# Optimization experiments

Hardware: AMD Instinct MI355X
Metric: run time of the kernel (lower is better)

The kernel has to match this reference:

```python
import jax, jax.numpy as jnp
import numpy as np

# Deformable Conv v2 (modulated) config matching init_kwargs
KH, KW = 3, 3
STRIDE = (1, 1)
PAD = (1, 1)
DIL = (1, 1)


def _deform_conv2d(input, offset, mask, weight, bias):
    """Modulated deformable conv2d (DCNv2), deformable_groups=1.

    input:  [B, C, H, W]
    offset: [B, 2*K, Ho, Wo]  (y, x) interleaved per kernel tap
    mask:   [B, K, Ho, Wo]
    weight: [O, C, KH, KW]
    bias:   [O]
    """
    B, C, H, W = input.shape
    O = weight.shape[0]
    K = KH * KW
    sh, sw = STRIDE
    ph, pw = PAD
    dh, dw = DIL
    Ho = (H + 2 * ph - dh * (KH - 1) - 1) // sh + 1
    Wo = (W + 2 * pw - dw * (KW - 1) - 1) // sw + 1
    dt = input.dtype

    # Base sampling grid per kernel tap: [K, Ho, Wo] (broadcasted)
    ky, kx = jnp.meshgrid(jnp.arange(KH), jnp.arange(KW), indexing='ij')
    ky = ky.reshape(K).astype(dt)
    kx = kx.reshape(K).astype(dt)
    base_y = (jnp.arange(Ho, dtype=dt) * sh - ph)[None, :, None] + (ky * dh)[:, None, None]
    base_x = (jnp.arange(Wo, dtype=dt) * sw - pw)[None, None, :] + (kx * dw)[:, None, None]

    off = offset.reshape(B, K, 2, Ho, Wo)
    y = base_y[None] + off[:, :, 0]  # [B, K, Ho, Wo]
    x = base_x[None] + off[:, :, 1]

    y0 = jnp.floor(y)
    x0 = jnp.floor(x)
    wy = y - y0  # fractional parts
    wx = x - x0

    flat = input.reshape(B, C, H * W)

    def gather(yi, xi):
        # zero padding outside the image
        valid = ((yi >= 0) & (yi < H) & (xi >= 0) & (xi < W)).astype(dt)
        yc = jnp.clip(yi, 0, H - 1).astype(jnp.int32)
        xc = jnp.clip(xi, 0, W - 1).astype(jnp.int32)
        idx = (yc * W + xc).reshape(B, 1, K * Ho * Wo)
        v = jnp.take_along_axis(flat, jnp.broadcast_to(idx, (B, C, K * Ho * Wo)), axis=2)
        return v.reshape(B, C, K, Ho, Wo) * valid[:, None]

    g00 = gather(y0, x0)
    g01 = gather(y0, x0 + 1)
    g10 = gather(y0 + 1, x0)
    g11 = gather(y0 + 1, x0 + 1)

    wy = wy[:, None]  # [B, 1, K, Ho, Wo]
    wx = wx[:, None]
    val = (g00 * (1 - wy) * (1 - wx) + g01 * (1 - wy) * wx
           + g10 * wy * (1 - wx) + g11 * wy * wx)
    val = val * mask[:, None]  # modulation

    out = jnp.einsum('bckq,ock->boq', val.reshape(B, C, K, Ho * Wo),
                     weight.reshape(O, C, K))
    return out.reshape(B, O, Ho, Wo) + bias[None, :, None, None]


def setup_inputs() -> dict:
    key = jax.random.key(0)
    k1, k2, k3, k4, k5 = jax.random.split(key, 5)
    B, C, H, W = 8, 64, 96, 96
    O = 64
    K = KH * KW
    input = jax.random.normal(k1, (B, C, H, W), dtype=jnp.float32)
    offset = jax.random.normal(k2, (B, 2 * K, H, W), dtype=jnp.float32)
    mask = jax.random.uniform(k3, (B, K, H, W), dtype=jnp.float32)
    fan_in = C * KH * KW
    bound = 1.0 / np.sqrt(fan_in)
    weight = jax.random.uniform(k4, (O, C, KH, KW), minval=-bound, maxval=bound, dtype=jnp.float32)
    bias = jax.random.uniform(k5, (O,), minval=-bound, maxval=bound, dtype=jnp.float32)
    return {"input": input, "offset": offset, "mask": mask, "weight": weight, "bias": bias}


def reference(input, offset, mask, weight, bias):
    return _deform_conv2d(input, offset, mask, weight, bias)
```

## Files before the change

kernel.cpp:

```cpp
#include <hip/hip_runtime.h>
#include <stdint.h>

#define Hs 96
#define Ws 96
#define HW 9216

typedef _Float16 h2 __attribute__((ext_vector_type(2)));
typedef _Float16 f16x8 __attribute__((ext_vector_type(8)));
typedef float f32x4 __attribute__((ext_vector_type(4)));

__device__ __forceinline__ unsigned interp4(h2 w00, h2 w01, h2 w10, h2 w11,
                                            unsigned a, unsigned bq, unsigned c,
                                            unsigned d) {
  h2 r = w00 * __builtin_bit_cast(h2, a) + w01 * __builtin_bit_cast(h2, bq) +
         w10 * __builtin_bit_cast(h2, c) + w11 * __builtin_bit_cast(h2, d);
  return __builtin_bit_cast(unsigned, r);
}

__global__ __launch_bounds__(256) void k_transpose(const float* __restrict__ in,
                                                   _Float16* __restrict__ cl) {
  __shared__ _Float16 lt[32 * 68];
  int tid = threadIdx.x;
  int blk = blockIdx.x;
  int xt = blk % 3;
  int r = blk / 3;
  int y = r % Hs;
  int b = r / Hs;
  int x0 = xt * 32;
  {
    int xx = tid & 31, cc = tid >> 5;
    const float* src = in + (size_t)b * 64 * HW + y * Ws + x0 + xx;
#pragma unroll
    for (int i = 0; i < 8; ++i) {
      int c = cc * 8 + i;
      lt[xx * 68 + c] = (_Float16)src[(size_t)c * HW];
    }
  }
  __syncthreads();
  {
    int c4 = tid & 15, pg = tid >> 4;
    _Float16* dst = cl + ((size_t)(b * Hs + y) * Ws + x0) * 64 + c4 * 4;
#pragma unroll
    for (int i = 0; i < 2; ++i) {
      int x = pg * 2 + i;
      *(uint2*)(dst + (size_t)x * 64) = *(const uint2*)(lt + x * 68 + c4 * 4);
    }
  }
}

__global__ __launch_bounds__(576) void k_wconv(const float* __restrict__ w,
                                               _Float16* __restrict__ wg) {
  int o = blockIdx.x;
  int r = threadIdx.x;
  int t = r >> 6, c = r & 63;
  wg[((size_t)(t * 8 + (c >> 3)) * 64 + o) * 8 + (c & 7)] =
      (_Float16)w[(o * 64 + c) * 9 + t];
}

__device__ __forceinline__ void sample_tap(const char* inb,
                                           const unsigned* preA,
                                           const uint2* preW, uint4* vrow,
                                           int t, int g, int j) {
#pragma unroll
  for (int it = 0; it < 2; ++it) {
    int gg = g + it * 32;
    unsigned ax = preA[t * 64 + gg];
    uint2 pw = preW[t * 64 + gg];
    int a00 = (int)(ax & ~127u) + j * 16;
    int a01 = a00 + ((ax & 1) << 7);
    int a10 = a00 + ((ax & 2) * 6144);
    int a11 = a10 + ((ax & 1) << 7);
    h2 w00 = __builtin_bit_cast(h2, __builtin_amdgcn_perm(pw.x, pw.x, 0x01000100u));
    h2 w01 = __builtin_bit_cast(h2, __builtin_amdgcn_perm(pw.x, pw.x, 0x03020302u));
    h2 w10 = __builtin_bit_cast(h2, __builtin_amdgcn_perm(pw.y, pw.y, 0x01000100u));
    h2 w11 = __builtin_bit_cast(h2, __builtin_amdgcn_perm(pw.y, pw.y, 0x03020302u));
    uint4 g00 = *(const uint4*)(inb + a00);
    uint4 g01 = *(const uint4*)(inb + a01);
    uint4 g10 = *(const uint4*)(inb + a10);
    uint4 g11 = *(const uint4*)(inb + a11);
    uint4 o;
    o.x = interp4(w00, w01, w10, w11, g00.x, g01.x, g10.x, g11.x);
    o.y = interp4(w00, w01, w10, w11, g00.y, g01.y, g10.y, g11.y);
    o.z = interp4(w00, w01, w10, w11, g00.z, g01.z, g10.z, g11.z);
    o.w = interp4(w00, w01, w10, w11, g00.w, g01.w, g10.w, g11.w);
    vrow[gg * 9 + j] = o;
  }
}

__global__ __launch_bounds__(256, 5) void k_fused(
    const _Float16* __restrict__ incl, const float* __restrict__ off,
    const float* __restrict__ msk, const _Float16* __restrict__ wg,
    const float* __restrict__ bias, float* __restrict__ out) {
  __shared__ unsigned preA[576];
  __shared__ uint2 preW[576];
  __shared__ uint4 Vb[2][64 * 9];

  int tid = threadIdx.x;
  int blk = blockIdx.x;
  int b = blk & 7;
  int q0 = (blk >> 3) * 64;

  for (int i = tid; i < 576; i += 256) {
    int t = i >> 6, p = i & 63;
    int q = q0 + p;
    int qy = (int)(((unsigned)q * 43691u) >> 22);
    int qx = q - qy * 96;
    int ty = t / 3, tx = t - ty * 3;
    float dy = off[(size_t)(b * 18 + 2 * t) * HW + q];
    float dx = off[(size_t)(b * 18 + 2 * t + 1) * HW + q];
    float mv = msk[(size_t)(b * 9 + t) * HW + q];
    float yf = (float)(qy - 1 + ty) + dy;
    float xf = (float)(qx - 1 + tx) + dx;
    float y0f = floorf(yf), x0f = floorf(xf);
    float wy = yf - y0f, wx = xf - x0f;
    int y0 = (int)y0f, x0i = (int)x0f;
    int y1 = y0 + 1, x1 = x0i + 1;
    bool yv0 = (y0 >= 0) && (y0 < Hs);
    bool yv1 = (y1 >= 0) && (y1 < Hs);
    bool xv0 = (x0i >= 0) && (x0i < Ws);
    bool xv1 = (x1 >= 0) && (x1 < Ws);
    int y0c = min(max(y0, 0), Hs - 1), y1c = min(max(y1, 0), Hs - 1);
    int x0c = min(max(x0i, 0), Ws - 1), x1c = min(max(x1, 0), Ws - 1);
    float omy = 1.f - wy, omx = 1.f - wx;
    float f00 = omy * omx * mv * ((yv0 && xv0) ? 1.f : 0.f);
    float f01 = omy * wx  * mv * ((yv0 && xv1) ? 1.f : 0.f);
    float f10 = wy  * omx * mv * ((yv1 && xv0) ? 1.f : 0.f);
    float f11 = wy  * wx  * mv * ((yv1 && xv1) ? 1.f : 0.f);
    preA[i] = ((unsigned)(b * HW + y0c * 96 + x0c) * 128u) |
              (unsigned)(x1c - x0c) | ((unsigned)(y1c - y0c) << 1);
    uint2 pw;
    pw.x = __builtin_bit_cast(unsigned, __builtin_amdgcn_cvt_pkrtz(f00, f01));
    pw.y = __builtin_bit_cast(unsigned, __builtin_amdgcn_cvt_pkrtz(f10, f11));
    preW[i] = pw;
  }
  __syncthreads();

  int j = tid & 7;
  int g = tid >> 3;
  int lane = tid & 63, wv = tid >> 6;
  int n16 = lane & 15, q4 = lane >> 4;
  const char* inb = (const char*)incl;
  const uint4* Ag = (const uint4*)wg;

  f32x4 acc[4];
#pragma unroll
  for (int mt = 0; mt < 4; ++mt) {
    f32x4 z = {0.f, 0.f, 0.f, 0.f};
    acc[mt] = z;
  }

  sample_tap(inb, preA, preW, &Vb[0][0], 0, g, j);
  __syncthreads();

  for (int t = 0; t < 9; ++t) {
    int buf = t & 1;
    if (t < 8)
      sample_tap(inb, preA, preW, &Vb[buf ^ 1][0], t + 1, g, j);
#pragma unroll
    for (int kc = 0; kc < 2; ++kc) {
      f16x8 bfr = __builtin_bit_cast(
          f16x8, Vb[buf][(wv * 16 + n16) * 9 + kc * 4 + q4]);
#pragma unroll
      for (int mt = 0; mt < 4; ++mt) {
        f16x8 afr = __builtin_bit_cast(
            f16x8, Ag[(size_t)((t * 8 + kc * 4 + q4) * 64 + mt * 16 + n16)]);
        acc[mt] = __builtin_amdgcn_mfma_f32_16x16x32_f16(afr, bfr, acc[mt],
                                                         0, 0, 0);
      }
    }
    __syncthreads();
  }

  int colq = q0 + wv * 16 + n16;
  float* op = out + (size_t)b * 64 * HW + colq;
#pragma unroll
  for (int mt = 0; mt < 4; ++mt)
#pragma unroll
    for (int r = 0; r < 4; ++r) {
      int m = mt * 16 + q4 * 4 + r;
      op[(size_t)m * HW] = acc[mt][r] + bias[m];
    }
}

extern "C" void kernel_launch(void* const* d_in, const int* in_sizes, int n_in,
                              void* d_out, int out_size, void* d_ws, size_t ws_size,
                              hipStream_t stream) {
  const float* input = (const float*)d_in[0];
  const float* offset = (const float*)d_in[1];
  const float* mask = (const float*)d_in[2];
  const float* weight = (const float*)d_in[3];
  const float* bias = (const float*)d_in[4];
  float* out = (float*)d_out;

  _Float16* incl = (_Float16*)d_ws;
  _Float16* wg = (_Float16*)((char*)d_ws + 9437184);

  k_transpose<<<dim3(2304), dim3(256), 0, stream>>>(input, incl);
  k_wconv<<<dim3(64), dim3(576), 0, stream>>>(weight, wg);
  k_fused<<<dim3(1152), dim3(256), 0, stream>>>(incl, offset, mask, wg, bias, out);
}
```

Baseline: 108.8 us.

## Software-pipeline gathers in registers and repartition MFMA work by output channel

The fused kernel now issues the next tap's bilinear gather loads into registers right after the barrier, so they overlap the current tap's MFMA work. The interpolation is then done and stored to LDS at the start of the next iteration instead of immediately. The MFMA split changes from each wave owning 16 pixels across all 64 output channels to each wave owning 16 output channels across all 64 pixels. Weight fragments are prefetched one tap ahead and bias loads are hoisted. This costs more live registers (launch bounds drop from 5 to 4 blocks per CU) and adds LDS reads of the B fragments per wave.

```diff
diff --git a/kernel.cpp b/kernel.cpp
--- a/kernel.cpp
+++ b/kernel.cpp
@@ -57,37 +57,7 @@
       (_Float16)w[(o * 64 + c) * 9 + t];
 }
 
-__device__ __forceinline__ void sample_tap(const char* inb,
-                                           const unsigned* preA,
-                                           const uint2* preW, uint4* vrow,
-                                           int t, int g, int j) {
-#pragma unroll
-  for (int it = 0; it < 2; ++it) {
-    int gg = g + it * 32;
-    unsigned ax = preA[t * 64 + gg];
-    uint2 pw = preW[t * 64 + gg];
-    int a00 = (int)(ax & ~127u) + j * 16;
-    int a01 = a00 + ((ax & 1) << 7);
-    int a10 = a00 + ((ax & 2) * 6144);
-    int a11 = a10 + ((ax & 1) << 7);
-    h2 w00 = __builtin_bit_cast(h2, __builtin_amdgcn_perm(pw.x, pw.x, 0x01000100u));
-    h2 w01 = __builtin_bit_cast(h2, __builtin_amdgcn_perm(pw.x, pw.x, 0x03020302u));
-    h2 w10 = __builtin_bit_cast(h2, __builtin_amdgcn_perm(pw.y, pw.y, 0x01000100u));
-    h2 w11 = __builtin_bit_cast(h2, __builtin_amdgcn_perm(pw.y, pw.y, 0x03020302u));
-    uint4 g00 = *(const uint4*)(inb + a00);
-    uint4 g01 = *(const uint4*)(inb + a01);
-    uint4 g10 = *(const uint4*)(inb + a10);
-    uint4 g11 = *(const uint4*)(inb + a11);
-    uint4 o;
-    o.x = interp4(w00, w01, w10, w11, g00.x, g01.x, g10.x, g11.x);
-    o.y = interp4(w00, w01, w10, w11, g00.y, g01.y, g10.y, g11.y);
-    o.z = interp4(w00, w01, w10, w11, g00.z, g01.z, g10.z, g11.z);
-    o.w = interp4(w00, w01, w10, w11, g00.w, g01.w, g10.w, g11.w);
-    vrow[gg * 9 + j] = o;
-  }
-}
-
-__global__ __launch_bounds__(256, 5) void k_fused(
+__global__ __launch_bounds__(256, 4) void k_fused(
     const _Float16* __restrict__ incl, const float* __restrict__ off,
     const float* __restrict__ msk, const _Float16* __restrict__ wg,
     const float* __restrict__ bias, float* __restrict__ out) {
@@ -141,45 +111,88 @@
   int n16 = lane & 15, q4 = lane >> 4;
   const char* inb = (const char*)incl;
   const uint4* Ag = (const uint4*)wg;
+  int arow = wv * 16 + n16;
 
   f32x4 acc[4];
 #pragma unroll
-  for (int mt = 0; mt < 4; ++mt) {
+  for (int pg = 0; pg < 4; ++pg) {
     f32x4 z = {0.f, 0.f, 0.f, 0.f};
-    acc[mt] = z;
-  }
-
-  sample_tap(inb, preA, preW, &Vb[0][0], 0, g, j);
-  __syncthreads();
-
+    acc[pg] = z;
+  }
+
+  uint4 ga[2][4];
+  uint4 afn0, afn1;
+
+#define ISSUE_GATHERS(T)                                                     \
+  _Pragma("unroll") for (int it = 0; it < 2; ++it) {                         \
+    int gg = g + it * 32;                                                    \
+    unsigned ax = preA[(T) * 64 + gg];                                       \
+    int a00 = (int)(ax & ~127u) + j * 16;                                    \
+    int a01 = a00 + ((ax & 1) << 7);                                         \
+    int a10 = a00 + ((ax & 2) * 6144);                                       \
+    int a11 = a10 + ((ax & 1) << 7);                                         \
+    ga[it][0] = *(const uint4*)(inb + a00);                                  \
+    ga[it][1] = *(const uint4*)(inb + a01);                                  \
+    ga[it][2] = *(const uint4*)(inb + a10);                                  \
+    ga[it][3] = *(const uint4*)(inb + a11);                                  \
+  }
+
+  ISSUE_GATHERS(0)
+  afn0 = Ag[(size_t)((0 + q4) * 64 + arow)];
+  afn1 = Ag[(size_t)((4 + q4) * 64 + arow)];
+
+#pragma unroll
   for (int t = 0; t < 9; ++t) {
     int buf = t & 1;
-    if (t < 8)
-      sample_tap(inb, preA, preW, &Vb[buf ^ 1][0], t + 1, g, j);
-#pragma unroll
-    for (int kc = 0; kc < 2; ++kc) {
-      f16x8 bfr = __builtin_bit_cast(
-          f16x8, Vb[buf][(wv * 16 + n16) * 9 + kc * 4 + q4]);
-#pragma unroll
-      for (int mt = 0; mt < 4; ++mt) {
-        f16x8 afr = __builtin_bit_cast(
-            f16x8, Ag[(size_t)((t * 8 + kc * 4 + q4) * 64 + mt * 16 + n16)]);
-        acc[mt] = __builtin_amdgcn_mfma_f32_16x16x32_f16(afr, bfr, acc[mt],
-                                                         0, 0, 0);
-      }
-    }
+    uint4 v0, v1;
+#pragma unroll
+    for (int it = 0; it < 2; ++it) {
+      int gg = g + it * 32;
+      uint2 pw = preW[t * 64 + gg];
+      h2 w00 = __builtin_bit_cast(h2, __builtin_amdgcn_perm(pw.x, pw.x, 0x01000100u));
+      h2 w01 = __builtin_bit_cast(h2, __builtin_amdgcn_perm(pw.x, pw.x, 0x03020302u));
+      h2 w10 = __builtin_bit_cast(h2, __builtin_amdgcn_perm(pw.y, pw.y, 0x01000100u));
+      h2 w11 = __builtin_bit_cast(h2, __builtin_amdgcn_perm(pw.y, pw.y, 0x03020302u));
+      uint4 r;
+      r.x = interp4(w00, w01, w10, w11, ga[it][0].x, ga[it][1].x, ga[it][2].x, ga[it][3].x);
+      r.y = interp4(w00, w01, w10, w11, ga[it][0].y, ga[it][1].y, ga[it][2].y, ga[it][3].y);
+      r.z = interp4(w00, w01, w10, w11, ga[it][0].z, ga[it][1].z, ga[it][2].z, ga[it][3].z);
+      r.w = interp4(w00, w01, w10, w11, ga[it][0].w, ga[it][1].w, ga[it][2].w, ga[it][3].w);
+      if (it == 0) v0 = r; else v1 = r;
+    }
+    uint4 afc0 = afn0, afc1 = afn1;
+    Vb[buf][g * 9 + j] = v0;
+    Vb[buf][(g + 32) * 9 + j] = v1;
     __syncthreads();
-  }
-
-  int colq = q0 + wv * 16 + n16;
-  float* op = out + (size_t)b * 64 * HW + colq;
-#pragma unroll
-  for (int mt = 0; mt < 4; ++mt)
-#pragma unroll
-    for (int r = 0; r < 4; ++r) {
-      int m = mt * 16 + q4 * 4 + r;
-      op[(size_t)m * HW] = acc[mt][r] + bias[m];
-    }
+    if (t < 8) {
+      ISSUE_GATHERS(t + 1)
+      afn0 = Ag[(size_t)(((t + 1) * 8 + q4) * 64 + arow)];
+      afn1 = Ag[(size_t)(((t + 1) * 8 + 4 + q4) * 64 + arow)];
+    }
+#pragma unroll
+    for (int pg = 0; pg < 4; ++pg) {
+      f16x8 b0 = __builtin_bit_cast(f16x8, Vb[buf][(pg * 16 + n16) * 9 + q4]);
+      f16x8 b1 = __builtin_bit_cast(f16x8, Vb[buf][(pg * 16 + n16) * 9 + 4 + q4]);
+      acc[pg] = __builtin_amdgcn_mfma_f32_16x16x32_f16(
+          __builtin_bit_cast(f16x8, afc0), b0, acc[pg], 0, 0, 0);
+      acc[pg] = __builtin_amdgcn_mfma_f32_16x16x32_f16(
+          __builtin_bit_cast(f16x8, afc1), b1, acc[pg], 0, 0, 0);
+    }
+  }
+#undef ISSUE_GATHERS
+
+  int m0 = wv * 16 + q4 * 4;
+  float bv[4];
+#pragma unroll
+  for (int r = 0; r < 4; ++r) bv[r] = bias[m0 + r];
+#pragma unroll
+  for (int pg = 0; pg < 4; ++pg) {
+    int col = q0 + pg * 16 + n16;
+    float* op = out + (size_t)b * 64 * HW + col;
+#pragma unroll
+    for (int r = 0; r < 4; ++r)
+      op[(size_t)(m0 + r) * HW] = acc[pg][r] + bv[r];
+  }
 }
 
 extern "C" void kernel_launch(void* const* d_in, const int* in_sizes, int n_in,
```

Result: faster. 102.1 us (-6.2%).
